# Optimization experiments

Measured on AMD Instinct MI355X. Metric: run time of the kernel, lower is better.

The kernel has to match this reference:

```python
import jax, jax.numpy as jnp
import numpy as np
from jax.scipy.linalg import expm

N = 2048
B = 16384
S = 0.1  # Euler step size s


def _A_hat(Theta):
    # row-softmax of Theta
    A = jax.nn.softmax(Theta, axis=1)
    # zero_diag=True path: mask diagonal, renormalize rows (guard empty rows)
    mask = 1.0 - jnp.eye(N, dtype=Theta.dtype)
    A = A * mask
    rs = jnp.sum(A, axis=1, keepdims=True)
    rs = jnp.where(rs > 0, rs, jnp.ones_like(rs))
    return A / rs


def setup_inputs() -> dict:
    key = jax.random.key(0)
    k1, k2 = jax.random.split(key)
    x = jax.random.normal(k1, (B, N), dtype=jnp.float32)
    # kaiming_uniform_(a=0) on [N,N]: bound = sqrt(6 / N)
    bound = float(np.sqrt(6.0 / N))
    Theta = jax.random.uniform(k2, (N, N), dtype=jnp.float32, minval=-bound, maxval=bound)
    return {"x": x, "Theta": Theta}


def reference(x, Theta):
    A = _A_hat(Theta)
    L = jnp.eye(N, dtype=Theta.dtype) - A          # normalized Laplacian
    M = expm(-S * L)                               # scaling-and-squaring matrix exp
    return x @ M.T                                 # [B, N]
```

## Files before the change

kernel.cpp:

```cpp
#include <hip/hip_runtime.h>
#include <hip/hip_bf16.h>
#include <cstdint>
#include <cstddef>

typedef unsigned short u16;
typedef unsigned int u32;
typedef __attribute__((ext_vector_type(8))) short bf16x8;
typedef __attribute__((ext_vector_type(4))) float f32x4;

#define ND 2048
#define BD 16384

#define C0 0.9048374180359595f
#define C1 0.09048374180359595f
#define C2 0.004524187090179798f
#define C3 1.5080623633932658e-4f
#define C4 3.770155908483165e-6f

__device__ __forceinline__ u16 f2bf(float f) {
  union { float f; u32 u; } v; v.f = f;
  u32 x = v.u;
  return (u16)((x + 0x7fffu + ((x >> 16) & 1u)) >> 16);
}

__device__ __forceinline__ void cp16(const void* g, void* l) {
  __builtin_amdgcn_global_load_lds(
      (const __attribute__((address_space(1))) u32*)g,
      (__attribute__((address_space(3))) u32*)l, 16, 0, 0);
}

__global__ void cvt_x(const float* __restrict__ in, u16* __restrict__ out) {
  const size_t i = ((size_t)blockIdx.x * 256 + threadIdx.x) * 8;
  float4 a = ((const float4*)(in + i))[0];
  float4 b = ((const float4*)(in + i))[1];
  union { u16 u[8]; uint4 v; } o;
  o.u[0] = f2bf(a.x); o.u[1] = f2bf(a.y); o.u[2] = f2bf(a.z); o.u[3] = f2bf(a.w);
  o.u[4] = f2bf(b.x); o.u[5] = f2bf(b.y); o.u[6] = f2bf(b.z); o.u[7] = f2bf(b.w);
  *((uint4*)(out + i)) = o.v;
}

__global__ void row_softmax(const float* __restrict__ Theta,
                            float* __restrict__ Rf, u16* __restrict__ Abf) {
  const int row = blockIdx.x;
  const int t = threadIdx.x;
  const float* tr = Theta + (size_t)row * ND;
  const int j0 = t * 8;
  float4 v0 = ((const float4*)tr)[t * 2];
  float4 v1 = ((const float4*)tr)[t * 2 + 1];
  float vals[8] = {v0.x, v0.y, v0.z, v0.w, v1.x, v1.y, v1.z, v1.w};

  float mx = -1e30f;
#pragma unroll
  for (int j = 0; j < 8; ++j)
    if (j0 + j != row) mx = fmaxf(mx, vals[j]);
#pragma unroll
  for (int o = 32; o > 0; o >>= 1) mx = fmaxf(mx, __shfl_xor(mx, o, 64));

  __shared__ float redm[4], reds[4];
  const int wv = t >> 6, ln = t & 63;
  if (ln == 0) redm[wv] = mx;
  __syncthreads();
  mx = fmaxf(fmaxf(redm[0], redm[1]), fmaxf(redm[2], redm[3]));

  float e[8];
  float s = 0.f;
#pragma unroll
  for (int j = 0; j < 8; ++j) {
    e[j] = (j0 + j == row) ? 0.f : expf(vals[j] - mx);
    s += e[j];
  }
#pragma unroll
  for (int o = 32; o > 0; o >>= 1) s += __shfl_xor(s, o, 64);
  if (ln == 0) reds[wv] = s;
  __syncthreads();
  s = reds[0] + reds[1] + reds[2] + reds[3];
  const float inv = 1.0f / s;

  float4 r0, r1;
  union { u16 u[8]; uint4 v; } ab;
  float a[8];
#pragma unroll
  for (int j = 0; j < 8; ++j) { a[j] = e[j] * inv; ab.u[j] = f2bf(a[j]); }
  r0 = make_float4(C1 * a[0], C1 * a[1], C1 * a[2], C1 * a[3]);
  r1 = make_float4(C1 * a[4], C1 * a[5], C1 * a[6], C1 * a[7]);
  float* rrow = Rf + (size_t)row * ND;
  ((float4*)rrow)[t * 2] = r0;
  ((float4*)rrow)[t * 2 + 1] = r1;
  *((uint4*)(Abf + (size_t)row * ND + j0)) = ab.v;
}

__global__ void transpose_bf16(const u16* __restrict__ in, u16* __restrict__ out) {
  __shared__ u16 tile[64][65];
  const int bx = blockIdx.x & 31, by = blockIdx.x >> 5;
  const int x = threadIdx.x & 63, y0 = threadIdx.x >> 6;
#pragma unroll
  for (int yy = y0; yy < 64; yy += 4)
    tile[yy][x] = in[(size_t)(by * 64 + yy) * ND + bx * 64 + x];
  __syncthreads();
#pragma unroll
  for (int yy = y0; yy < 64; yy += 4)
    out[(size_t)(bx * 64 + yy) * ND + by * 64 + x] = tile[x][yy];
}

template <int BM, int BN, int MODE>
__global__ void gemm_nt(const u16* __restrict__ Ag, const u16* __restrict__ Bg,
                        float* __restrict__ Fo, u16* __restrict__ Bo,
                        const float* __restrict__ Xf,
                        int M, int N, int K, float coef, int gridn) {
  constexpr int BK = 32;
  constexpr int FM = BM / 32;
  constexpr int FN = BN / 32;
  constexpr int CHA = (BM * BK) / (8 * 256);
  constexpr int CHB = (BN * BK) / (8 * 256);

  __shared__ u16 lA[2][BM * BK];
  __shared__ u16 lB[2][BN * BK];

  const int tid = threadIdx.x;
  const int lane = tid & 63;
  const int wave = tid >> 6;
  const int wm = wave >> 1;
  const int wn = wave & 1;
  const int lr = lane & 15;
  const int lk = (lane >> 4) << 3;

  const int nwg = gridDim.x;
  const int bid = blockIdx.x;
  const int swz = (bid & 7) * (nwg >> 3) + (bid >> 3);
  const int bm = swz / gridn;
  const int bn = swz % gridn;

  const u16* Abase = Ag + (size_t)bm * BM * K;
  const u16* Bbase = Bg + (size_t)bn * BN * K;

  f32x4 acc[FM][FN];
#pragma unroll
  for (int i = 0; i < FM; ++i)
#pragma unroll
    for (int j = 0; j < FN; ++j)
      acc[i][j] = (f32x4){0.f, 0.f, 0.f, 0.f};

  auto stage = [&](int buf, int k0) {
#pragma unroll
    for (int q = 0; q < CHA; ++q) {
      int c = q * 256 + tid;
      int row = c >> 2;
      int col = (c & 3) << 3;
      cp16(Abase + (size_t)row * K + k0 + col, &lA[buf][c * 8]);
    }
#pragma unroll
    for (int q = 0; q < CHB; ++q) {
      int c = q * 256 + tid;
      int row = c >> 2;
      int col = (c & 3) << 3;
      cp16(Bbase + (size_t)row * K + k0 + col, &lB[buf][c * 8]);
    }
  };

  const int NT = K >> 5;
  stage(0, 0);
  __syncthreads();
  int cur = 0;
  for (int t = 0; t < NT; ++t) {
    if (t + 1 < NT) stage(cur ^ 1, (t + 1) * BK);
    bf16x8 af[FM], bg[FN];
#pragma unroll
    for (int m = 0; m < FM; ++m)
      af[m] = *(const bf16x8*)&lA[cur][(wm * (BM / 2) + m * 16 + lr) * BK + lk];
#pragma unroll
    for (int n = 0; n < FN; ++n)
      bg[n] = *(const bf16x8*)&lB[cur][(wn * (BN / 2) + n * 16 + lr) * BK + lk];
#pragma unroll
    for (int m = 0; m < FM; ++m)
#pragma unroll
      for (int n = 0; n < FN; ++n)
        acc[m][n] = __builtin_amdgcn_mfma_f32_16x16x32_bf16(af[m], bg[n], acc[m][n], 0, 0, 0);
    __syncthreads();
    cur ^= 1;
  }

#pragma unroll
  for (int m = 0; m < FM; ++m) {
    const int grow0 = bm * BM + wm * (BM / 2) + m * 16 + ((lane >> 4) << 2);
#pragma unroll
    for (int n = 0; n < FN; ++n) {
      const int gcol = bn * BN + wn * (BN / 2) + n * 16 + lr;
#pragma unroll
      for (int r = 0; r < 4; ++r) {
        const size_t idx = (size_t)(grow0 + r) * N + gcol;
        const float v = acc[m][n][r];
        if (MODE == 0) {
          float nr = Fo[idx] + coef * v;
          Fo[idx] = nr;
          Bo[idx] = f2bf(v);
        } else if (MODE == 1) {
          Bo[idx] = f2bf(Fo[idx] + coef * v);
        } else {
          Fo[idx] = coef * Xf[idx] + v;
        }
      }
    }
  }
}

extern "C" void kernel_launch(void* const* d_in, const int* in_sizes, int n_in,
                              void* d_out, int out_size, void* d_ws, size_t ws_size,
                              hipStream_t stream) {
  const float* x = (const float*)d_in[0];
  const float* Theta = (const float*)d_in[1];
  float* out = (float*)d_out;

  char* ws = (char*)d_ws;
  u16* xbf   = (u16*)(ws);
  u16* Abf   = (u16*)(ws + 67108864);
  u16* Atbf  = (u16*)(ws + 75497472);
  u16* P2    = (u16*)(ws + 83886080);
  u16* Rbf   = (u16*)(ws + 92274688);
  float* Rf  = (float*)(ws + 100663296);

  cvt_x<<<dim3(16384), dim3(256), 0, stream>>>(x, xbf);
  row_softmax<<<dim3(2048), dim3(256), 0, stream>>>(Theta, Rf, Abf);
  transpose_bf16<<<dim3(1024), dim3(256), 0, stream>>>(Abf, Atbf);
  gemm_nt<64, 64, 0><<<dim3(1024), dim3(256), 0, stream>>>(
      Abf, Atbf, Rf, P2, nullptr, ND, ND, ND, C2, 32);
  gemm_nt<64, 64, 0><<<dim3(1024), dim3(256), 0, stream>>>(
      P2, Atbf, Rf, Abf, nullptr, ND, ND, ND, C3, 32);
  gemm_nt<64, 64, 1><<<dim3(1024), dim3(256), 0, stream>>>(
      Abf, Atbf, Rf, Rbf, nullptr, ND, ND, ND, C4, 32);
  gemm_nt<128, 128, 2><<<dim3(2048), dim3(256), 0, stream>>>(
      xbf, Rbf, out, nullptr, x, BD, ND, ND, C0, 16);
}
```

Measured before the change: 530.7 us.

## Factor Taylor polynomial via Horner, use triple-buffered deep-tile GEMMs

The degree-4 Taylor series for the matrix exponential is reorganised so that it needs two N×N GEMMs plus an extra transpose instead of three sequential A-power GEMMs. The first GEMM computes A² and a fused T = C2·I + C3·A + C4·A², and the second computes C1·A + A²·T. The fp32 R accumulator buffer is removed and its terms are recomputed from bf16 inputs in the GEMM epilogues, which adds some bf16 rounding risk. The GEMM kernel gains triple-buffered LDS with manual vmcnt waits, setprio around the MFMA loop, a k-major LDS layout, and larger tiles (256×256 with 512 threads for the big x·Rᵀ GEMM), aiming to reduce load stalls and improve reuse.

New measurement: 635.6 us. 19.8% more time.

```diff
diff --git a/kernel.cpp b/kernel.cpp
--- a/kernel.cpp
+++ b/kernel.cpp
@@ -21,6 +21,10 @@
   union { float f; u32 u; } v; v.f = f;
   u32 x = v.u;
   return (u16)((x + 0x7fffu + ((x >> 16) & 1u)) >> 16);
+}
+
+__device__ __forceinline__ float bf2f(u16 b) {
+  union { u32 u; float f; } v; v.u = ((u32)b) << 16; return v.f;
 }
 
 __device__ __forceinline__ void cp16(const void* g, void* l) {
@@ -39,8 +43,7 @@
   *((uint4*)(out + i)) = o.v;
 }
 
-__global__ void row_softmax(const float* __restrict__ Theta,
-                            float* __restrict__ Rf, u16* __restrict__ Abf) {
+__global__ void row_softmax(const float* __restrict__ Theta, u16* __restrict__ Abf) {
   const int row = blockIdx.x;
   const int t = threadIdx.x;
   const float* tr = Theta + (size_t)row * ND;
@@ -76,16 +79,9 @@
   s = reds[0] + reds[1] + reds[2] + reds[3];
   const float inv = 1.0f / s;
 
-  float4 r0, r1;
   union { u16 u[8]; uint4 v; } ab;
-  float a[8];
-#pragma unroll
-  for (int j = 0; j < 8; ++j) { a[j] = e[j] * inv; ab.u[j] = f2bf(a[j]); }
-  r0 = make_float4(C1 * a[0], C1 * a[1], C1 * a[2], C1 * a[3]);
-  r1 = make_float4(C1 * a[4], C1 * a[5], C1 * a[6], C1 * a[7]);
-  float* rrow = Rf + (size_t)row * ND;
-  ((float4*)rrow)[t * 2] = r0;
-  ((float4*)rrow)[t * 2 + 1] = r1;
+#pragma unroll
+  for (int j = 0; j < 8; ++j) ab.u[j] = f2bf(e[j] * inv);
   *((uint4*)(Abf + (size_t)row * ND + j0)) = ab.v;
 }
 
@@ -102,27 +98,29 @@
     out[(size_t)(bx * 64 + yy) * ND + by * 64 + x] = tile[x][yy];
 }
 
-template <int BM, int BN, int MODE>
-__global__ void gemm_nt(const u16* __restrict__ Ag, const u16* __restrict__ Bg,
-                        float* __restrict__ Fo, u16* __restrict__ Bo,
-                        const float* __restrict__ Xf,
-                        int M, int N, int K, float coef, int gridn) {
-  constexpr int BK = 32;
-  constexpr int FM = BM / 32;
-  constexpr int FN = BN / 32;
-  constexpr int CHA = (BM * BK) / (8 * 256);
-  constexpr int CHB = (BN * BK) / (8 * 256);
-
-  __shared__ u16 lA[2][BM * BK];
-  __shared__ u16 lB[2][BN * BK];
+template <int BM, int BN, int WM, int WN, int THREADS, int MODE>
+__global__ __launch_bounds__(THREADS, 2) void gemm_deep(
+    const u16* __restrict__ Ag, const u16* __restrict__ Bg,
+    float* __restrict__ Fo, u16* __restrict__ Bo, u16* __restrict__ Bo2,
+    const u16* __restrict__ Aux, const float* __restrict__ Xf,
+    int Nn, int K, int gridn) {
+  constexpr int LOGM = (BM == 256) ? 8 : 7;
+  constexpr int LOGN = (BN == 256) ? 8 : 7;
+  constexpr int FM = BM / WM / 16;
+  constexpr int FN = BN / WN / 16;
+  constexpr int CHA = BM * 4 / THREADS;
+  constexpr int CHB = BN * 4 / THREADS;
+
+  __shared__ u16 lA[3][BM * 32];
+  __shared__ u16 lB[3][BN * 32];
 
   const int tid = threadIdx.x;
   const int lane = tid & 63;
   const int wave = tid >> 6;
-  const int wm = wave >> 1;
-  const int wn = wave & 1;
+  const int wm = wave / WN;
+  const int wn = wave % WN;
   const int lr = lane & 15;
-  const int lk = (lane >> 4) << 3;
+  const int kc = lane >> 4;
 
   const int nwg = gridDim.x;
   const int bid = blockIdx.x;
@@ -140,63 +138,81 @@
     for (int j = 0; j < FN; ++j)
       acc[i][j] = (f32x4){0.f, 0.f, 0.f, 0.f};
 
-  auto stage = [&](int buf, int k0) {
+  auto stage = [&](int s, int kt) {
+    const int kbase = kt * 32;
 #pragma unroll
     for (int q = 0; q < CHA; ++q) {
-      int c = q * 256 + tid;
-      int row = c >> 2;
-      int col = (c & 3) << 3;
-      cp16(Abase + (size_t)row * K + k0 + col, &lA[buf][c * 8]);
+      int c = q * THREADS + tid;
+      int kcc = c >> LOGM, row = c & (BM - 1);
+      cp16(Abase + (size_t)row * K + kbase + kcc * 8, &lA[s][c * 8]);
     }
 #pragma unroll
     for (int q = 0; q < CHB; ++q) {
-      int c = q * 256 + tid;
-      int row = c >> 2;
-      int col = (c & 3) << 3;
-      cp16(Bbase + (size_t)row * K + k0 + col, &lB[buf][c * 8]);
-    }
+      int c = q * THREADS + tid;
+      int kcc = c >> LOGN, col = c & (BN - 1);
+      cp16(Bbase + (size_t)col * K + kbase + kcc * 8, &lB[s][c * 8]);
+    }
+  };
+
+  auto compute = [&](int s) {
+    bf16x8 af[FM], bg[FN];
+#pragma unroll
+    for (int m = 0; m < FM; ++m) {
+      int row = wm * (BM / WM) + m * 16 + lr;
+      af[m] = *(const bf16x8*)&lA[s][(kc * BM + row) * 8];
+    }
+#pragma unroll
+    for (int n = 0; n < FN; ++n) {
+      int col = wn * (BN / WN) + n * 16 + lr;
+      bg[n] = *(const bf16x8*)&lB[s][(kc * BN + col) * 8];
+    }
+    __builtin_amdgcn_s_setprio(1);
+#pragma unroll
+    for (int m = 0; m < FM; ++m)
+#pragma unroll
+      for (int n = 0; n < FN; ++n)
+        acc[m][n] = __builtin_amdgcn_mfma_f32_16x16x32_bf16(af[m], bg[n], acc[m][n], 0, 0, 0);
+    __builtin_amdgcn_s_setprio(0);
   };
 
   const int NT = K >> 5;
   stage(0, 0);
-  __syncthreads();
-  int cur = 0;
-  for (int t = 0; t < NT; ++t) {
-    if (t + 1 < NT) stage(cur ^ 1, (t + 1) * BK);
-    bf16x8 af[FM], bg[FN];
-#pragma unroll
-    for (int m = 0; m < FM; ++m)
-      af[m] = *(const bf16x8*)&lA[cur][(wm * (BM / 2) + m * 16 + lr) * BK + lk];
-#pragma unroll
-    for (int n = 0; n < FN; ++n)
-      bg[n] = *(const bf16x8*)&lB[cur][(wn * (BN / 2) + n * 16 + lr) * BK + lk];
-#pragma unroll
-    for (int m = 0; m < FM; ++m)
-#pragma unroll
-      for (int n = 0; n < FN; ++n)
-        acc[m][n] = __builtin_amdgcn_mfma_f32_16x16x32_bf16(af[m], bg[n], acc[m][n], 0, 0, 0);
-    __syncthreads();
-    cur ^= 1;
+  stage(1, 1);
+  for (int t = 0; t < NT - 2; ++t) {
+    stage((t + 2) % 3, t + 2);
+    asm volatile("s_waitcnt vmcnt(8)" ::: "memory");
+    __builtin_amdgcn_s_barrier();
+    compute(t % 3);
+    __builtin_amdgcn_s_barrier();
   }
-
+  asm volatile("s_waitcnt vmcnt(4)" ::: "memory");
+  __builtin_amdgcn_s_barrier();
+  compute((NT - 2) % 3);
+  __builtin_amdgcn_s_barrier();
+  asm volatile("s_waitcnt vmcnt(0)" ::: "memory");
+  __builtin_amdgcn_s_barrier();
+  compute((NT - 1) % 3);
+
+  const int r0 = (lane >> 4) << 2;
 #pragma unroll
   for (int m = 0; m < FM; ++m) {
-    const int grow0 = bm * BM + wm * (BM / 2) + m * 16 + ((lane >> 4) << 2);
+    const int grow0 = bm * BM + wm * (BM / WM) + m * 16 + r0;
 #pragma unroll
     for (int n = 0; n < FN; ++n) {
-      const int gcol = bn * BN + wn * (BN / 2) + n * 16 + lr;
+      const int gcol = bn * BN + wn * (BN / WN) + n * 16 + lr;
 #pragma unroll
       for (int r = 0; r < 4; ++r) {
-        const size_t idx = (size_t)(grow0 + r) * N + gcol;
+        const int grow = grow0 + r;
+        const size_t idx = (size_t)grow * Nn + gcol;
         const float v = acc[m][n][r];
-        if (MODE == 0) {
-          float nr = Fo[idx] + coef * v;
-          Fo[idx] = nr;
+        if (MODE == 3) {
           Bo[idx] = f2bf(v);
+          float tv = ((grow == gcol) ? C2 : 0.0f) + C3 * bf2f(Aux[idx]) + C4 * v;
+          Bo2[idx] = f2bf(tv);
         } else if (MODE == 1) {
-          Bo[idx] = f2bf(Fo[idx] + coef * v);
+          Bo[idx] = f2bf(C1 * bf2f(Aux[idx]) + v);
         } else {
-          Fo[idx] = coef * Xf[idx] + v;
+          Fo[idx] = C0 * Xf[idx] + v;
         }
       }
     }
@@ -211,22 +227,22 @@
   float* out = (float*)d_out;
 
   char* ws = (char*)d_ws;
-  u16* xbf   = (u16*)(ws);
-  u16* Abf   = (u16*)(ws + 67108864);
-  u16* Atbf  = (u16*)(ws + 75497472);
-  u16* P2    = (u16*)(ws + 83886080);
-  u16* Rbf   = (u16*)(ws + 92274688);
-  float* Rf  = (float*)(ws + 100663296);
+  u16* xbf  = (u16*)(ws);
+  u16* Abf  = (u16*)(ws + 67108864);
+  u16* Atbf = (u16*)(ws + 75497472);
+  u16* P2   = (u16*)(ws + 83886080);
+  u16* Tbf  = (u16*)(ws + 92274688);
+  u16* Ttbf = (u16*)(ws + 100663296);
+  u16* Rbf  = (u16*)(ws + 109051904);
 
   cvt_x<<<dim3(16384), dim3(256), 0, stream>>>(x, xbf);
-  row_softmax<<<dim3(2048), dim3(256), 0, stream>>>(Theta, Rf, Abf);
+  row_softmax<<<dim3(2048), dim3(256), 0, stream>>>(Theta, Abf);
   transpose_bf16<<<dim3(1024), dim3(256), 0, stream>>>(Abf, Atbf);
-  gemm_nt<64, 64, 0><<<dim3(1024), dim3(256), 0, stream>>>(
-      Abf, Atbf, Rf, P2, nullptr, ND, ND, ND, C2, 32);
-  gemm_nt<64, 64, 0><<<dim3(1024), dim3(256), 0, stream>>>(
-      P2, Atbf, Rf, Abf, nullptr, ND, ND, ND, C3, 32);
-  gemm_nt<64, 64, 1><<<dim3(1024), dim3(256), 0, stream>>>(
-      Abf, Atbf, Rf, Rbf, nullptr, ND, ND, ND, C4, 32);
-  gemm_nt<128, 128, 2><<<dim3(2048), dim3(256), 0, stream>>>(
-      xbf, Rbf, out, nullptr, x, BD, ND, ND, C0, 16);
-}
+  gemm_deep<128, 128, 2, 2, 256, 3><<<dim3(256), dim3(256), 0, stream>>>(
+      Abf, Atbf, nullptr, P2, Tbf, Abf, nullptr, ND, ND, 16);
+  transpose_bf16<<<dim3(1024), dim3(256), 0, stream>>>(Tbf, Ttbf);
+  gemm_deep<128, 128, 2, 2, 256, 1><<<dim3(256), dim3(256), 0, stream>>>(
+      P2, Ttbf, nullptr, Rbf, nullptr, Abf, nullptr, ND, ND, 16);
+  gemm_deep<256, 256, 2, 4, 512, 2><<<dim3(512), dim3(512), 0, stream>>>(
+      xbf, Rbf, out, nullptr, nullptr, nullptr, x, ND, ND, 8);
+}
```
